# Performance work log

Measured on AMD Instinct MI355X. Metric: run time of the kernel, lower is better.

Reference implementation:

```python
import jax, jax.numpy as jnp
import numpy as np

GROUPS = 32
EPS = 1e-5


def group_norm(x, w, b):
    B, C, H, W = x.shape
    xg = x.reshape(B, GROUPS, C // GROUPS, H, W)
    mu = xg.mean(axis=(2, 3, 4), keepdims=True)
    var = xg.var(axis=(2, 3, 4), keepdims=True)
    xg = (xg - mu) * jax.lax.rsqrt(var + EPS)
    return xg.reshape(B, C, H, W) * w[None, :, None, None] + b[None, :, None, None]


def conv1x1(x, w, b):
    # 1x1 conv == per-position GEMM over channels
    return jnp.einsum('bchw,dc->bdhw', x, w) + b[None, :, None, None]


def setup_inputs() -> dict:
    key = jax.random.key(0)
    ks = jax.random.split(key, 8)
    B, C, H, W = 16, 512, 32, 32
    scale = C ** -0.5  # keep pre-softmax logits well-conditioned
    return {
        'x': jax.random.normal(ks[0], (B, C, H, W), jnp.float32),
        'temb': jax.random.normal(ks[1], (B, C), jnp.float32),
        'gn_w': jnp.ones((C,), jnp.float32),
        'gn_b': jnp.zeros((C,), jnp.float32),
        'q_w': jax.random.normal(ks[2], (C, C), jnp.float32) * scale,
        'q_b': jnp.zeros((C,), jnp.float32),
        'k_w': jax.random.normal(ks[3], (C, C), jnp.float32) * scale,
        'k_b': jnp.zeros((C,), jnp.float32),
        'v_w': jax.random.normal(ks[4], (C, C), jnp.float32) * scale,
        'v_b': jnp.zeros((C,), jnp.float32),
        'p_w': jax.random.normal(ks[5], (C, C), jnp.float32) * scale,
        'p_b': jnp.zeros((C,), jnp.float32),
    }


def reference(x, temb, gn_w, gn_b, q_w, q_b, k_w, k_b, v_w, v_b, p_w, p_b):
    B, C, H, W = x.shape
    h = group_norm(x, gn_w, gn_b)
    q = conv1x1(h, q_w, q_b)
    k = conv1x1(h, k_w, k_b)
    v = conv1x1(h, v_w, v_b)
    # spatial self-attention: every (h,w) query attends over all (H,W) keys
    scores = jnp.einsum('bchw,bcHW->bhwHW', q, k) * (C ** -0.5)  # [B,H,W,H,W]
    attn = jax.nn.softmax(scores.reshape(B, H, W, H * W), axis=-1).reshape(B, H, W, H, W)
    h = jnp.einsum('bhwHW,bcHW->bchw', attn, v)
    return x + conv1x1(h, p_w, p_b)
```

## Files before the change

kernel.cpp:

```cpp
#include <hip/hip_runtime.h>

typedef unsigned short u16;
typedef __bf16 bf16x8 __attribute__((ext_vector_type(8)));
typedef float f32x4 __attribute__((ext_vector_type(4)));
typedef unsigned short u16x8 __attribute__((ext_vector_type(8)));

__device__ __forceinline__ u16 f2bf(float f) {
  unsigned u = __builtin_bit_cast(unsigned, f);
  u += 0x7fffu + ((u >> 16) & 1u);
  return (u16)(u >> 16);
}
__device__ __forceinline__ float b2f(u16 h) {
  return __builtin_bit_cast(float, (unsigned)h << 16);
}

__device__ __forceinline__ void async16(const void* g, void* l) {
  __builtin_amdgcn_global_load_lds((const __attribute__((address_space(1))) void*)g,
                                   (__attribute__((address_space(3))) void*)l, 16, 0, 0);
}

__global__ __launch_bounds__(256) void cvt_kernel(const float* __restrict__ qw, const float* __restrict__ kw,
                                                  const float* __restrict__ vw, const float* __restrict__ pw,
                                                  const float* __restrict__ qb, const float* __restrict__ kb,
                                                  u16* __restrict__ wqk, u16* __restrict__ wv,
                                                  u16* __restrict__ wp, float* __restrict__ qkb,
                                                  float scale) {
  if (blockIdx.y == 4) {
    int i = blockIdx.x * 256 + threadIdx.x;
    if (i < 512) qkb[i] = qb[i] * scale;
    else if (i < 1024) qkb[i] = kb[i - 512];
    return;
  }
  const float* s;
  u16* o;
  float sc = 1.f;
  switch (blockIdx.y) {
    case 0: s = qw; o = wqk; sc = scale; break;
    case 1: s = kw; o = wqk + 262144; break;
    case 2: s = vw; o = wv; break;
    default: s = pw; o = wp; break;
  }
  int i = (blockIdx.x * 256 + threadIdx.x) * 4;
  float4 v = *(const float4*)(s + i);
  ushort4 pk = { f2bf(v.x * sc), f2bf(v.y * sc), f2bf(v.z * sc), f2bf(v.w * sc) };
  *(ushort4*)&o[i] = pk;
}

#define GN_ROW 1026

__global__ __launch_bounds__(256) void gn_kernel(const float* __restrict__ x, const float* __restrict__ w,
                                                 const float* __restrict__ bias, u16* __restrict__ hn) {
  __shared__ u16 tile[16 * GN_ROW];
  __shared__ float red[18];
  const int tid = threadIdx.x;
  const int bb = blockIdx.x >> 5;
  const int g = blockIdx.x & 31;
  const float4* xb = (const float4*)(x + ((size_t)bb * 512 + (size_t)g * 16) * 1024);

  float s = 0.f, sq = 0.f;
#pragma unroll
  for (int j = 0; j < 16; ++j) {
    float4 v = xb[j * 256 + tid];
    s += v.x + v.y + v.z + v.w;
    sq += v.x * v.x + v.y * v.y + v.z * v.z + v.w * v.w;
    int base = j * GN_ROW + tid * 4;
    ushort2 p0 = { f2bf(v.x), f2bf(v.y) };
    ushort2 p1 = { f2bf(v.z), f2bf(v.w) };
    *(ushort2*)&tile[base] = p0;
    *(ushort2*)&tile[base + 2] = p1;
  }
#pragma unroll
  for (int o = 32; o; o >>= 1) {
    s += __shfl_down(s, o, 64);
    sq += __shfl_down(sq, o, 64);
  }
  const int wv = tid >> 6;
  if ((tid & 63) == 0) { red[wv] = s; red[wv + 4] = sq; }
  __syncthreads();
  if (tid == 0) {
    float S = red[0] + red[1] + red[2] + red[3];
    float Q = red[4] + red[5] + red[6] + red[7];
    float mean = S * (1.f / 16384.f);
    float var = Q * (1.f / 16384.f) - mean * mean;
    red[16] = mean;
    red[17] = rsqrtf(var + 1e-5f);
  }
  __syncthreads();
  const float mean = red[16], rstd = red[17];
  const int c0 = g * 16;

  float wf[16], bf_[16];
#pragma unroll
  for (int c = 0; c < 16; ++c) {
    float wc = w[c0 + c];
    wf[c] = wc * rstd;
    bf_[c] = bias[c0 + c] - mean * rstd * wc;
  }
#pragma unroll
  for (int it = 0; it < 4; ++it) {
    int hw = it * 256 + tid;
    u16x8 lo{}, hi{};
#pragma unroll
    for (int c = 0; c < 8; ++c) {
      lo[c] = f2bf(b2f(tile[c * GN_ROW + hw]) * wf[c] + bf_[c]);
      hi[c] = f2bf(b2f(tile[(c + 8) * GN_ROW + hw]) * wf[c + 8] + bf_[c + 8]);
    }
    u16* dst = hn + ((size_t)bb * 1024 + hw) * 512 + c0;
    *(u16x8*)dst = lo;
    *(u16x8*)(dst + 8) = hi;
  }
}

template <typename OutT>
__global__ __launch_bounds__(256) void gemm_nt(const u16* __restrict__ A, const u16* __restrict__ Bt,
                                               OutT* __restrict__ C, const float* __restrict__ bias_m,
                                               const float* __restrict__ bias_n, const float* __restrict__ res,
                                               int K, int lda, int ldb, int ldc,
                                               size_t sA, size_t sB, size_t sC, size_t sRes,
                                               int T, int lognbx) {
  __shared__ u16 lsA[128 * 64];
  __shared__ u16 lsB[128 * 64];
  int fi = blockIdx.x;
  const int halfT = T << 3;
  const int h = (fi >= halfT);
  fi -= h * halfT;
  const int tile = fi >> 3;
  const int zb = (fi & 7) + (h << 3);
  const int bx = tile & ((1 << lognbx) - 1);
  const int by = tile >> lognbx;

  const int tid = threadIdx.x;
  const int lane = tid & 63;
  const int wave = tid >> 6;
  const int wm = wave >> 1, wn = wave & 1;
  const int tm = by * 128, tn = bx * 128;
  const u16* Ab = A + (size_t)zb * sA;
  const u16* Bb = Bt + (size_t)zb * sB;

  f32x4 acc[4][4] = {};
  const int q = lane >> 4, r = lane & 15;

  int srow[4], gch[4];
#pragma unroll
  for (int i = 0; i < 4; ++i) {
    int e = tid + i * 256;
    srow[i] = e >> 3;
    gch[i] = (e & 7) ^ (srow[i] & 7);
  }

  for (int k0 = 0; k0 < K; k0 += 64) {
    __syncthreads();
#pragma unroll
    for (int i = 0; i < 4; ++i) {
      async16(Ab + (size_t)(tm + srow[i]) * lda + k0 + gch[i] * 8, (char*)lsA + (tid + i * 256) * 16);
      async16(Bb + (size_t)(tn + srow[i]) * ldb + k0 + gch[i] * 8, (char*)lsB + (tid + i * 256) * 16);
    }
    __syncthreads();

#pragma unroll
    for (int kk = 0; kk < 2; ++kk) {
      bf16x8 af[4], bfv[4];
#pragma unroll
      for (int mt = 0; mt < 4; ++mt) {
        int row = wm * 64 + mt * 16 + r;
        int chunk = (kk * 4 + q) ^ (row & 7);
        af[mt] = *(const bf16x8*)(const void*)&lsA[row * 64 + chunk * 8];
      }
#pragma unroll
      for (int nt = 0; nt < 4; ++nt) {
        int row = wn * 64 + nt * 16 + r;
        int chunk = (kk * 4 + q) ^ (row & 7);
        bfv[nt] = *(const bf16x8*)(const void*)&lsB[row * 64 + chunk * 8];
      }
#pragma unroll
      for (int mt = 0; mt < 4; ++mt)
#pragma unroll
        for (int nt = 0; nt < 4; ++nt)
          acc[mt][nt] = __builtin_amdgcn_mfma_f32_16x16x32_bf16(af[mt], bfv[nt], acc[mt][nt], 0, 0, 0);
    }
  }

  OutT* Cb = C + (size_t)zb * sC;
  const float* Rb = res ? res + (size_t)zb * sRes : nullptr;
#pragma unroll
  for (int mt = 0; mt < 4; ++mt) {
#pragma unroll
    for (int nt = 0; nt < 4; ++nt) {
      const int col = tn + wn * 64 + nt * 16 + r;
      const float bn = bias_n ? bias_n[col] : 0.f;
#pragma unroll
      for (int reg = 0; reg < 4; ++reg) {
        const int row = tm + wm * 64 + mt * 16 + q * 4 + reg;
        float v = acc[mt][nt][reg];
        const float bm = bias_m ? bias_m[row] : 0.f;
        v = v + bm + bn;
        const size_t idx = (size_t)row * ldc + col;
        if (Rb) v += Rb[idx];
        if constexpr (__is_same(OutT, u16)) Cb[idx] = f2bf(v);
        else Cb[idx] = v;
      }
    }
  }
}

__global__ __launch_bounds__(256) void softmax_kernel(u16* __restrict__ S) {
  const int row = blockIdx.x * 4 + (threadIdx.x >> 6);
  const int lane = threadIdx.x & 63;
  u16* p = S + (size_t)row * 1024;
  u16x8 a = *(const u16x8*)(p + lane * 8);
  u16x8 b = *(const u16x8*)(p + 512 + lane * 8);
  float va[8], vb[8];
  float m = -3.0e38f;
#pragma unroll
  for (int j = 0; j < 8; ++j) {
    va[j] = b2f(a[j]);
    vb[j] = b2f(b[j]);
    m = fmaxf(m, fmaxf(va[j], vb[j]));
  }
#pragma unroll
  for (int o = 32; o; o >>= 1) m = fmaxf(m, __shfl_xor(m, o, 64));
  float s = 0.f;
#pragma unroll
  for (int j = 0; j < 8; ++j) {
    va[j] = __expf(va[j] - m);
    vb[j] = __expf(vb[j] - m);
    s += va[j] + vb[j];
  }
#pragma unroll
  for (int o = 32; o; o >>= 1) s += __shfl_xor(s, o, 64);
  const float inv = 1.f / s;
  u16x8 oa, ob;
#pragma unroll
  for (int j = 0; j < 8; ++j) {
    oa[j] = f2bf(va[j] * inv);
    ob[j] = f2bf(vb[j] * inv);
  }
  *(u16x8*)(p + lane * 8) = oa;
  *(u16x8*)(p + 512 + lane * 8) = ob;
}

extern "C" void kernel_launch(void* const* d_in, const int* in_sizes, int n_in,
                              void* d_out, int out_size, void* d_ws, size_t ws_size,
                              hipStream_t stream) {
  const float* x = (const float*)d_in[0];
  const float* gn_w = (const float*)d_in[2];
  const float* gn_b = (const float*)d_in[3];
  const float* q_w = (const float*)d_in[4];
  const float* q_b = (const float*)d_in[5];
  const float* k_w = (const float*)d_in[6];
  const float* k_b = (const float*)d_in[7];
  const float* v_w = (const float*)d_in[8];
  const float* v_b = (const float*)d_in[9];
  const float* p_w = (const float*)d_in[10];
  const float* p_b = (const float*)d_in[11];
  float* out = (float*)d_out;

  u16* wqk = (u16*)d_ws;
  u16* wv = wqk + 524288;
  u16* wp = wv + 262144;
  float* qkb = (float*)(wp + 262144);
  u16* hn = wp + 262144 + 2048;
  u16* qkt = hn + 8388608;
  u16* vv = qkt + 16777216;
  u16* ot = vv + 8388608;
  u16* Sb = ot + 8388608;

  const float inv_sqrt_c = 0.044194173824159216f;
  const size_t sHN = 524288, sS = 1048576;

  cvt_kernel<<<dim3(256, 5), 256, 0, stream>>>(q_w, k_w, v_w, p_w, q_b, k_b, wqk, wv, wp, qkb, inv_sqrt_c);
  gn_kernel<<<512, 256, 0, stream>>>(x, gn_w, gn_b, hn);

  gemm_nt<u16><<<dim3(16 * 64), 256, 0, stream>>>(hn, wqk, qkt, nullptr, qkb, nullptr,
                                                  512, 512, 512, 1024, sHN, 0, sS, 0, 64, 3);
  gemm_nt<u16><<<dim3(16 * 32), 256, 0, stream>>>(wv, hn, vv, v_b, nullptr, nullptr,
                                                  512, 512, 512, 1024, 0, sHN, sHN, 0, 32, 3);
  gemm_nt<u16><<<dim3(16 * 64), 256, 0, stream>>>(qkt, qkt + 512, Sb, nullptr, nullptr, nullptr,
                                                  512, 1024, 1024, 1024, sS, sS, sS, 0, 64, 3);
  softmax_kernel<<<4096, 256, 0, stream>>>(Sb);
  gemm_nt<u16><<<dim3(16 * 32), 256, 0, stream>>>(Sb, vv, ot, nullptr, nullptr, nullptr,
                                                  1024, 1024, 1024, 512, sS, sHN, sHN, 0, 32, 2);
  gemm_nt<float><<<dim3(16 * 32), 256, 0, stream>>>(wp, ot, out, p_b, nullptr, x,
                                                    512, 512, 512, 1024, 0, sHN, sHN, sHN, 32, 3);
}
```

Before: 276.0 us.

## Template GEMM on tile shape and use larger 512-thread tiles with nontemporal epilogue

Makes the bf16 MFMA GEMM templated on block tile sizes and the wave layout. All five GEMMs now launch 512-thread blocks with 256x256 or 128x256 tiles instead of 128x128 tiles, which raises operand reuse per LDS load and cuts redundant global reads. The epilogue's residual reads and output writes become nontemporal. The trade-off is fewer blocks (one per CU), higher register and LDS use per block, and less latency hiding, since the loop is still single-buffered.

Result: slower. 359.1 us (+30.1%).

```diff
diff --git a/kernel.cpp b/kernel.cpp
--- a/kernel.cpp
+++ b/kernel.cpp
@@ -111,15 +111,21 @@
   }
 }
 
-template <typename OutT>
-__global__ __launch_bounds__(256) void gemm_nt(const u16* __restrict__ A, const u16* __restrict__ Bt,
-                                               OutT* __restrict__ C, const float* __restrict__ bias_m,
-                                               const float* __restrict__ bias_n, const float* __restrict__ res,
-                                               int K, int lda, int ldb, int ldc,
-                                               size_t sA, size_t sB, size_t sC, size_t sRes,
-                                               int T, int lognbx) {
-  __shared__ u16 lsA[128 * 64];
-  __shared__ u16 lsB[128 * 64];
+template <int BM, int BN, int WGN, typename OutT>
+__global__ __launch_bounds__(512, 2) void gemm_nt(const u16* __restrict__ A, const u16* __restrict__ Bt,
+                                                  OutT* __restrict__ C, const float* __restrict__ bias_m,
+                                                  const float* __restrict__ bias_n, const float* __restrict__ res,
+                                                  int K, int lda, int ldb, int ldc,
+                                                  size_t sA, size_t sB, size_t sC, size_t sRes,
+                                                  int T, int lognbx) {
+  constexpr int WGM = 8 / WGN;
+  constexpr int SUBN = BN / WGN;
+  constexpr int NT = SUBN / 16;
+  constexpr int AIT = BM * 8 / 512;
+  constexpr int BIT = BN * 8 / 512;
+  __shared__ u16 lsA[BM * 64];
+  __shared__ u16 lsB[BN * 64];
+
   int fi = blockIdx.x;
   const int halfT = T << 3;
   const int h = (fi >= halfT);
@@ -132,34 +138,41 @@
   const int tid = threadIdx.x;
   const int lane = tid & 63;
   const int wave = tid >> 6;
-  const int wm = wave >> 1, wn = wave & 1;
-  const int tm = by * 128, tn = bx * 128;
+  const int wm = wave / WGN, wn = wave % WGN;
+  const int tm = by * BM, tn = bx * BN;
   const u16* Ab = A + (size_t)zb * sA;
   const u16* Bb = Bt + (size_t)zb * sB;
 
-  f32x4 acc[4][4] = {};
+  f32x4 acc[4][NT] = {};
   const int q = lane >> 4, r = lane & 15;
 
-  int srow[4], gch[4];
-#pragma unroll
-  for (int i = 0; i < 4; ++i) {
-    int e = tid + i * 256;
-    srow[i] = e >> 3;
-    gch[i] = (e & 7) ^ (srow[i] & 7);
+  int arow[AIT], ach[AIT], brow[BIT], bch[BIT];
+#pragma unroll
+  for (int i = 0; i < AIT; ++i) {
+    int e = tid + i * 512;
+    arow[i] = e >> 3;
+    ach[i] = (e & 7) ^ (arow[i] & 7);
+  }
+#pragma unroll
+  for (int i = 0; i < BIT; ++i) {
+    int e = tid + i * 512;
+    brow[i] = e >> 3;
+    bch[i] = (e & 7) ^ (brow[i] & 7);
   }
 
   for (int k0 = 0; k0 < K; k0 += 64) {
     __syncthreads();
 #pragma unroll
-    for (int i = 0; i < 4; ++i) {
-      async16(Ab + (size_t)(tm + srow[i]) * lda + k0 + gch[i] * 8, (char*)lsA + (tid + i * 256) * 16);
-      async16(Bb + (size_t)(tn + srow[i]) * ldb + k0 + gch[i] * 8, (char*)lsB + (tid + i * 256) * 16);
-    }
+    for (int i = 0; i < AIT; ++i)
+      async16(Ab + (size_t)(tm + arow[i]) * lda + k0 + ach[i] * 8, (char*)lsA + (tid + i * 512) * 16);
+#pragma unroll
+    for (int i = 0; i < BIT; ++i)
+      async16(Bb + (size_t)(tn + brow[i]) * ldb + k0 + bch[i] * 8, (char*)lsB + (tid + i * 512) * 16);
     __syncthreads();
 
 #pragma unroll
     for (int kk = 0; kk < 2; ++kk) {
-      bf16x8 af[4], bfv[4];
+      bf16x8 af[4], bfv[NT];
 #pragma unroll
       for (int mt = 0; mt < 4; ++mt) {
         int row = wm * 64 + mt * 16 + r;
@@ -167,15 +180,15 @@
         af[mt] = *(const bf16x8*)(const void*)&lsA[row * 64 + chunk * 8];
       }
 #pragma unroll
-      for (int nt = 0; nt < 4; ++nt) {
-        int row = wn * 64 + nt * 16 + r;
+      for (int nt = 0; nt < NT; ++nt) {
+        int row = wn * SUBN + nt * 16 + r;
         int chunk = (kk * 4 + q) ^ (row & 7);
         bfv[nt] = *(const bf16x8*)(const void*)&lsB[row * 64 + chunk * 8];
       }
 #pragma unroll
       for (int mt = 0; mt < 4; ++mt)
 #pragma unroll
-        for (int nt = 0; nt < 4; ++nt)
+        for (int nt = 0; nt < NT; ++nt)
           acc[mt][nt] = __builtin_amdgcn_mfma_f32_16x16x32_bf16(af[mt], bfv[nt], acc[mt][nt], 0, 0, 0);
     }
   }
@@ -185,8 +198,8 @@
 #pragma unroll
   for (int mt = 0; mt < 4; ++mt) {
 #pragma unroll
-    for (int nt = 0; nt < 4; ++nt) {
-      const int col = tn + wn * 64 + nt * 16 + r;
+    for (int nt = 0; nt < NT; ++nt) {
+      const int col = tn + wn * SUBN + nt * 16 + r;
       const float bn = bias_n ? bias_n[col] : 0.f;
 #pragma unroll
       for (int reg = 0; reg < 4; ++reg) {
@@ -195,9 +208,9 @@
         const float bm = bias_m ? bias_m[row] : 0.f;
         v = v + bm + bn;
         const size_t idx = (size_t)row * ldc + col;
-        if (Rb) v += Rb[idx];
-        if constexpr (__is_same(OutT, u16)) Cb[idx] = f2bf(v);
-        else Cb[idx] = v;
+        if (Rb) v += __builtin_nontemporal_load(&Rb[idx]);
+        if constexpr (__is_same(OutT, u16)) __builtin_nontemporal_store(f2bf(v), &Cb[idx]);
+        else __builtin_nontemporal_store(v, &Cb[idx]);
       }
     }
   }
@@ -271,15 +284,15 @@
   cvt_kernel<<<dim3(256, 5), 256, 0, stream>>>(q_w, k_w, v_w, p_w, q_b, k_b, wqk, wv, wp, qkb, inv_sqrt_c);
   gn_kernel<<<512, 256, 0, stream>>>(x, gn_w, gn_b, hn);
 
-  gemm_nt<u16><<<dim3(16 * 64), 256, 0, stream>>>(hn, wqk, qkt, nullptr, qkb, nullptr,
-                                                  512, 512, 512, 1024, sHN, 0, sS, 0, 64, 3);
-  gemm_nt<u16><<<dim3(16 * 32), 256, 0, stream>>>(wv, hn, vv, v_b, nullptr, nullptr,
-                                                  512, 512, 512, 1024, 0, sHN, sHN, 0, 32, 3);
-  gemm_nt<u16><<<dim3(16 * 64), 256, 0, stream>>>(qkt, qkt + 512, Sb, nullptr, nullptr, nullptr,
-                                                  512, 1024, 1024, 1024, sS, sS, sS, 0, 64, 3);
+  gemm_nt<256, 256, 2, u16><<<256, 512, 0, stream>>>(hn, wqk, qkt, nullptr, qkb, nullptr,
+                                                     512, 512, 512, 1024, sHN, 0, sS, 0, 16, 2);
+  gemm_nt<128, 256, 4, u16><<<256, 512, 0, stream>>>(wv, hn, vv, v_b, nullptr, nullptr,
+                                                     512, 512, 512, 1024, 0, sHN, sHN, 0, 16, 2);
+  gemm_nt<256, 256, 2, u16><<<256, 512, 0, stream>>>(qkt, qkt + 512, Sb, nullptr, nullptr, nullptr,
+                                                     512, 1024, 1024, 1024, sS, sS, sS, 0, 16, 2);
   softmax_kernel<<<4096, 256, 0, stream>>>(Sb);
-  gemm_nt<u16><<<dim3(16 * 32), 256, 0, stream>>>(Sb, vv, ot, nullptr, nullptr, nullptr,
-                                                  1024, 1024, 1024, 512, sS, sHN, sHN, 0, 32, 2);
-  gemm_nt<float><<<dim3(16 * 32), 256, 0, stream>>>(wp, ot, out, p_b, nullptr, x,
-                                                    512, 512, 512, 1024, 0, sHN, sHN, sHN, 32, 3);
-}
+  gemm_nt<128, 256, 4, u16><<<256, 512, 0, stream>>>(Sb, vv, ot, nullptr, nullptr, nullptr,
+                                                     1024, 1024, 1024, 512, sS, sHN, sHN, 0, 16, 1);
+  gemm_nt<128, 256, 4, float><<<256, 512, 0, stream>>>(wp, ot, out, p_b, nullptr, x,
+                                                       512, 512, 512, 1024, 0, sHN, sHN, sHN, 16, 2);
+}
```

## Double-buffer LDS tiles in GEMM to overlap global loads with MFMA

Applied to the files above, without the earlier changes.

The GEMM mainloop now keeps two LDS buffers per operand and issues the async global-to-LDS loads for the next K-tile before computing the current one. Explicit vmcnt waits and raw s_barrier replace the two __syncthreads per iteration. This is meant to hide global memory latency behind MFMA work, at the cost of doubling LDS use to 64KB per block, which can lower occupancy. The hand-written waitcnt and barriers also risk ordering bugs if the compiler reorders LDS reads.

Measured after the change: 265.1 us. 4.0% less time.

```diff
diff --git a/kernel.cpp b/kernel.cpp
--- a/kernel.cpp
+++ b/kernel.cpp
@@ -118,8 +118,8 @@
                                                int K, int lda, int ldb, int ldc,
                                                size_t sA, size_t sB, size_t sC, size_t sRes,
                                                int T, int lognbx) {
-  __shared__ u16 lsA[128 * 64];
-  __shared__ u16 lsB[128 * 64];
+  __shared__ u16 lsA[2][128 * 64];
+  __shared__ u16 lsB[2][128 * 64];
   int fi = blockIdx.x;
   const int halfT = T << 3;
   const int h = (fi >= halfT);
@@ -148,15 +148,29 @@
     gch[i] = (e & 7) ^ (srow[i] & 7);
   }
 
-  for (int k0 = 0; k0 < K; k0 += 64) {
-    __syncthreads();
-#pragma unroll
-    for (int i = 0; i < 4; ++i) {
-      async16(Ab + (size_t)(tm + srow[i]) * lda + k0 + gch[i] * 8, (char*)lsA + (tid + i * 256) * 16);
-      async16(Bb + (size_t)(tn + srow[i]) * ldb + k0 + gch[i] * 8, (char*)lsB + (tid + i * 256) * 16);
+  auto stage = [&](int k0, int db) {
+#pragma unroll
+    for (int i = 0; i < 4; ++i)
+      async16(Ab + (size_t)(tm + srow[i]) * lda + k0 + gch[i] * 8, (char*)lsA[db] + (tid + i * 256) * 16);
+#pragma unroll
+    for (int i = 0; i < 4; ++i)
+      async16(Bb + (size_t)(tn + srow[i]) * ldb + k0 + gch[i] * 8, (char*)lsB[db] + (tid + i * 256) * 16);
+  };
+
+  const int nk = K >> 6;
+  stage(0, 0);
+  for (int k = 0; k < nk; ++k) {
+    const int cur = k & 1;
+    if (k + 1 < nk) {
+      stage((k + 1) << 6, cur ^ 1);
+      asm volatile("s_waitcnt vmcnt(8)" ::: "memory");
+    } else {
+      asm volatile("s_waitcnt vmcnt(0)" ::: "memory");
     }
-    __syncthreads();
-
+    asm volatile("s_barrier" ::: "memory");
+
+    const u16* As = lsA[cur];
+    const u16* Bs = lsB[cur];
 #pragma unroll
     for (int kk = 0; kk < 2; ++kk) {
       bf16x8 af[4], bfv[4];
@@ -164,13 +178,13 @@
       for (int mt = 0; mt < 4; ++mt) {
         int row = wm * 64 + mt * 16 + r;
         int chunk = (kk * 4 + q) ^ (row & 7);
-        af[mt] = *(const bf16x8*)(const void*)&lsA[row * 64 + chunk * 8];
+        af[mt] = *(const bf16x8*)(const void*)&As[row * 64 + chunk * 8];
       }
 #pragma unroll
       for (int nt = 0; nt < 4; ++nt) {
         int row = wn * 64 + nt * 16 + r;
         int chunk = (kk * 4 + q) ^ (row & 7);
-        bfv[nt] = *(const bf16x8*)(const void*)&lsB[row * 64 + chunk * 8];
+        bfv[nt] = *(const bf16x8*)(const void*)&Bs[row * 64 + chunk * 8];
       }
 #pragma unroll
       for (int mt = 0; mt < 4; ++mt)
@@ -178,6 +192,7 @@
         for (int nt = 0; nt < 4; ++nt)
           acc[mt][nt] = __builtin_amdgcn_mfma_f32_16x16x32_bf16(af[mt], bfv[nt], acc[mt][nt], 0, 0, 0);
     }
+    asm volatile("s_barrier" ::: "memory");
   }
 
   OutT* Cb = C + (size_t)zb * sC;
```

## Double-buffer GEMM shared tiles with register prefetch instead of direct global-to-LDS loads

Applied to the files above, without the earlier changes.

The GEMM main loop now stages tiles through registers into two shared-memory buffers with a K step of 32. The next tile's global loads are issued before the current tile's MFMAs and written to the other buffer afterwards, so each step needs one barrier instead of two. It also sets a minimum of 3 blocks per SM in launch bounds and switches to a new swizzle matched to the 32-wide rows. Costs are more registers for the prefetch and more loop iterations, each doing fewer MFMAs.

Result: faster. 264.5 us (-4.2%).

```diff
diff --git a/kernel.cpp b/kernel.cpp
--- a/kernel.cpp
+++ b/kernel.cpp
@@ -12,11 +12,6 @@
 }
 __device__ __forceinline__ float b2f(u16 h) {
   return __builtin_bit_cast(float, (unsigned)h << 16);
-}
-
-__device__ __forceinline__ void async16(const void* g, void* l) {
-  __builtin_amdgcn_global_load_lds((const __attribute__((address_space(1))) void*)g,
-                                   (__attribute__((address_space(3))) void*)l, 16, 0, 0);
 }
 
 __global__ __launch_bounds__(256) void cvt_kernel(const float* __restrict__ qw, const float* __restrict__ kw,
@@ -112,14 +107,14 @@
 }
 
 template <typename OutT>
-__global__ __launch_bounds__(256) void gemm_nt(const u16* __restrict__ A, const u16* __restrict__ Bt,
-                                               OutT* __restrict__ C, const float* __restrict__ bias_m,
-                                               const float* __restrict__ bias_n, const float* __restrict__ res,
-                                               int K, int lda, int ldb, int ldc,
-                                               size_t sA, size_t sB, size_t sC, size_t sRes,
-                                               int T, int lognbx) {
-  __shared__ u16 lsA[128 * 64];
-  __shared__ u16 lsB[128 * 64];
+__global__ __launch_bounds__(256, 3) void gemm_nt(const u16* __restrict__ A, const u16* __restrict__ Bt,
+                                                  OutT* __restrict__ C, const float* __restrict__ bias_m,
+                                                  const float* __restrict__ bias_n, const float* __restrict__ res,
+                                                  int K, int lda, int ldb, int ldc,
+                                                  size_t sA, size_t sB, size_t sC, size_t sRes,
+                                                  int T, int lognbx) {
+  __shared__ u16 lsA[2][128 * 32];
+  __shared__ u16 lsB[2][128 * 32];
   int fi = blockIdx.x;
   const int halfT = T << 3;
   const int h = (fi >= halfT);
@@ -140,44 +135,65 @@
   f32x4 acc[4][4] = {};
   const int q = lane >> 4, r = lane & 15;
 
-  int srow[4], gch[4];
-#pragma unroll
-  for (int i = 0; i < 4; ++i) {
-    int e = tid + i * 256;
-    srow[i] = e >> 3;
-    gch[i] = (e & 7) ^ (srow[i] & 7);
-  }
-
-  for (int k0 = 0; k0 < K; k0 += 64) {
+  const int ra = tid >> 2;
+  const int g = tid & 3;
+  const int s0 = g ^ ((ra >> 1) & 3);
+  const int s1 = g ^ (((ra + 64) >> 1) & 3);
+  const u16* pa0 = Ab + (size_t)(tm + ra) * lda + g * 8;
+  const u16* pa1 = Ab + (size_t)(tm + ra + 64) * lda + g * 8;
+  const u16* pb0 = Bb + (size_t)(tn + ra) * ldb + g * 8;
+  const u16* pb1 = Bb + (size_t)(tn + ra + 64) * ldb + g * 8;
+  const int wa0 = ra * 32 + s0 * 8, wa1 = (ra + 64) * 32 + s1 * 8;
+
+  u16x8 rA0, rA1, rB0, rB1;
+  rA0 = *(const u16x8*)(pa0);
+  rA1 = *(const u16x8*)(pa1);
+  rB0 = *(const u16x8*)(pb0);
+  rB1 = *(const u16x8*)(pb1);
+  *(u16x8*)&lsA[0][wa0] = rA0;
+  *(u16x8*)&lsA[0][wa1] = rA1;
+  *(u16x8*)&lsB[0][wa0] = rB0;
+  *(u16x8*)&lsB[0][wa1] = rB1;
+  __syncthreads();
+
+  int offA[4], offB[4];
+#pragma unroll
+  for (int mt = 0; mt < 4; ++mt) {
+    int rowa = wm * 64 + mt * 16 + r;
+    offA[mt] = rowa * 32 + (q ^ ((rowa >> 1) & 3)) * 8;
+    int rowb = wn * 64 + mt * 16 + r;
+    offB[mt] = rowb * 32 + (q ^ ((rowb >> 1) & 3)) * 8;
+  }
+
+  const int nk = K >> 5;
+  for (int k = 0; k < nk; ++k) {
+    const int cur = k & 1;
+    if (k + 1 < nk) {
+      const int k0 = (k + 1) << 5;
+      rA0 = *(const u16x8*)(pa0 + k0);
+      rA1 = *(const u16x8*)(pa1 + k0);
+      rB0 = *(const u16x8*)(pb0 + k0);
+      rB1 = *(const u16x8*)(pb1 + k0);
+    }
+    bf16x8 af[4], bfv[4];
+#pragma unroll
+    for (int mt = 0; mt < 4; ++mt) {
+      af[mt] = *(const bf16x8*)(const void*)&lsA[cur][offA[mt]];
+      bfv[mt] = *(const bf16x8*)(const void*)&lsB[cur][offB[mt]];
+    }
+#pragma unroll
+    for (int mt = 0; mt < 4; ++mt)
+#pragma unroll
+      for (int nt = 0; nt < 4; ++nt)
+        acc[mt][nt] = __builtin_amdgcn_mfma_f32_16x16x32_bf16(af[mt], bfv[nt], acc[mt][nt], 0, 0, 0);
+    if (k + 1 < nk) {
+      const int nxt = cur ^ 1;
+      *(u16x8*)&lsA[nxt][wa0] = rA0;
+      *(u16x8*)&lsA[nxt][wa1] = rA1;
+      *(u16x8*)&lsB[nxt][wa0] = rB0;
+      *(u16x8*)&lsB[nxt][wa1] = rB1;
+    }
     __syncthreads();
-#pragma unroll
-    for (int i = 0; i < 4; ++i) {
-      async16(Ab + (size_t)(tm + srow[i]) * lda + k0 + gch[i] * 8, (char*)lsA + (tid + i * 256) * 16);
-      async16(Bb + (size_t)(tn + srow[i]) * ldb + k0 + gch[i] * 8, (char*)lsB + (tid + i * 256) * 16);
-    }
-    __syncthreads();
-
-#pragma unroll
-    for (int kk = 0; kk < 2; ++kk) {
-      bf16x8 af[4], bfv[4];
-#pragma unroll
-      for (int mt = 0; mt < 4; ++mt) {
-        int row = wm * 64 + mt * 16 + r;
-        int chunk = (kk * 4 + q) ^ (row & 7);
-        af[mt] = *(const bf16x8*)(const void*)&lsA[row * 64 + chunk * 8];
-      }
-#pragma unroll
-      for (int nt = 0; nt < 4; ++nt) {
-        int row = wn * 64 + nt * 16 + r;
-        int chunk = (kk * 4 + q) ^ (row & 7);
-        bfv[nt] = *(const bf16x8*)(const void*)&lsB[row * 64 + chunk * 8];
-      }
-#pragma unroll
-      for (int mt = 0; mt < 4; ++mt)
-#pragma unroll
-        for (int nt = 0; nt < 4; ++nt)
-          acc[mt][nt] = __builtin_amdgcn_mfma_f32_16x16x32_bf16(af[mt], bfv[nt], acc[mt][nt], 0, 0, 0);
-    }
   }
 
   OutT* Cb = C + (size_t)zb * sC;
```
